# Optimization experiments

Measured on AMD Instinct MI355X. Metric: run time of the kernel, lower is better.

## Reference

```python
import jax, jax.numpy as jnp
import numpy as np

N_ENT = 50000
N_EDGE = 500000
H_DIM = 128
N_REL_TAB = 475  # 2*n_rel + 1


def setup_inputs() -> dict:
    key = jax.random.key(0)
    ks = jax.random.split(key, 8)
    scale = 1.0 / np.sqrt(H_DIM)
    return {
        "ent_emb": jax.random.normal(ks[0], (N_ENT, H_DIM), jnp.float32) * scale,
        "rel_emb": jax.random.normal(ks[1], (N_REL_TAB, H_DIM), jnp.float32) * scale,
        "w_edge": jax.random.normal(ks[2], (H_DIM, H_DIM), jnp.float32) * scale,
        "w_node": jax.random.normal(ks[3], (H_DIM, H_DIM), jnp.float32) * scale,
        "w_comp": jax.random.normal(ks[4], (H_DIM, H_DIM), jnp.float32) * scale,
        "src": jax.random.randint(ks[5], (N_EDGE,), 0, N_ENT, jnp.int32),
        "dst": jax.random.randint(ks[6], (N_EDGE,), 0, N_ENT, jnp.int32),
        "rel_id": jax.random.randint(ks[7], (N_EDGE,), 0, N_REL_TAB - 1, jnp.int32),
    }


def _edge_softmax(logits, dst, n_nodes):
    # dgl.ops.edge_softmax: softmax over incoming edges of each destination node
    m = jax.ops.segment_max(logits, dst, num_segments=n_nodes)  # (N,)
    ex = jnp.exp(logits - m[dst])                               # (E,)
    s = jax.ops.segment_sum(ex, dst, num_segments=n_nodes)     # (N,)
    return ex / s[dst]


def _attn_aggregate(msg, key_emb_dst, dst, n_nodes, w):
    # norm = e_dot_v, edge_softmax, weighted scatter-sum, GEMM, Tanh
    logits = jnp.sum(msg * key_emb_dst, axis=-1)                # (E,)
    a = _edge_softmax(logits, dst, n_nodes)                     # (E,)
    neigh = jax.ops.segment_sum(msg * a[:, None], dst, num_segments=n_nodes)  # (N,H)
    return jnp.tanh(neigh @ w)


def reference(ent_emb, rel_emb, w_edge, w_node, w_comp, src, dst, rel_id):
    n = ent_emb.shape[0]
    v = ent_emb[dst]            # (E,H) destination node emb (shared key for all layers)
    u = ent_emb[src]            # (E,H)
    r = rel_emb[rel_id]         # (E,H)

    # EdgeLayer: message = rel emb
    edge_out = _attn_aggregate(r, v, dst, n, w_edge)
    # NodeLayer: message = src node emb (u_dot_v logits, u_mul_e aggregation)
    node_out = _attn_aggregate(u, v, dst, n, w_node)
    # CompLayer (comp_op='add'): message = u + rel emb
    comp_out = _attn_aggregate(u + r, v, dst, n, w_comp)

    return ent_emb + edge_out + node_out + comp_out
```

## Files before the change

### kernel.cpp

```cpp
#include <hip/hip_runtime.h>
#include <math.h>

#define N_ENT   50000
#define N_EDGE  500000
#define HD      128

typedef unsigned int u32;
typedef __attribute__((ext_vector_type(8))) short short8;
typedef __attribute__((ext_vector_type(4))) float f32x4;
typedef __attribute__((ext_vector_type(4))) u32 u32x4;

__device__ __forceinline__ u32 bf16_1(float f) {
  u32 u = __float_as_uint(f);
  return (u + 0x7fffu + ((u >> 16) & 1u)) >> 16;
}
__device__ __forceinline__ u32 bf16_pack(float lo, float hi) {
  return bf16_1(lo) | (bf16_1(hi) << 16);
}
__device__ __forceinline__ float fast_tanh(float x) {
  float e = __expf(2.f * x);
  return 1.f - 2.f * __builtin_amdgcn_rcpf(e + 1.f);
}

__global__ void k_degree(const int* __restrict__ dst, int* __restrict__ counts) {
  int e = blockIdx.x * 256 + threadIdx.x;
  if (e < N_EDGE) atomicAdd(&counts[dst[e]], 1);
}

__global__ void k_blocksum(const int* __restrict__ counts, int* __restrict__ bsum) {
  __shared__ int sh[256];
  int i = blockIdx.x * 256 + threadIdx.x;
  sh[threadIdx.x] = (i < N_ENT) ? counts[i] : 0;
  __syncthreads();
  for (int off = 128; off > 0; off >>= 1) {
    if (threadIdx.x < off) sh[threadIdx.x] += sh[threadIdx.x + off];
    __syncthreads();
  }
  if (threadIdx.x == 0) bsum[blockIdx.x] = sh[0];
}

__global__ void k_scan_top(int* __restrict__ bsum, int nb) {
  __shared__ int sh[256];
  int t = threadIdx.x;
  int v = (t < nb) ? bsum[t] : 0;
  sh[t] = v;
  __syncthreads();
  for (int off = 1; off < 256; off <<= 1) {
    int x = (t >= off) ? sh[t - off] : 0;
    __syncthreads();
    sh[t] += x;
    __syncthreads();
  }
  if (t < nb) bsum[t] = sh[t] - v;
}

__global__ void k_scan_final(const int* __restrict__ counts, const int* __restrict__ bsum,
                             int* __restrict__ row_ptr) {
  __shared__ int sh[256];
  int t = threadIdx.x;
  int i = blockIdx.x * 256 + t;
  int v = (i < N_ENT) ? counts[i] : 0;
  sh[t] = v;
  __syncthreads();
  for (int off = 1; off < 256; off <<= 1) {
    int x = (t >= off) ? sh[t - off] : 0;
    __syncthreads();
    sh[t] += x;
    __syncthreads();
  }
  if (i < N_ENT) row_ptr[i] = sh[t] - v + bsum[blockIdx.x];
  if (i == N_ENT - 1) row_ptr[N_ENT] = N_EDGE;
}

__global__ void k_scatter(const int* __restrict__ src, const int* __restrict__ dst,
                          const int* __restrict__ rel, const int* __restrict__ row_ptr,
                          int* __restrict__ cursor, int2* __restrict__ psr) {
  int e = blockIdx.x * 256 + threadIdx.x;
  if (e >= N_EDGE) return;
  int d = dst[e];
  int pos = row_ptr[d] + atomicAdd(&cursor[d], 1);
  psr[pos] = make_int2(src[e], rel[e]);
}

__global__ __launch_bounds__(256) void k_aggregate(
    const float* __restrict__ ent, const float* __restrict__ rel,
    const int* __restrict__ row_ptr, const int2* __restrict__ psr,
    u32* __restrict__ neighb) {
  int lane = threadIdx.x & 63;
  int node = blockIdx.x * 4 + (threadIdx.x >> 6);
  int grp = lane >> 4, gl = lane & 15;

  const float* vp = ent + (size_t)node * HD + gl * 8;
  float4 va = *(const float4*)vp, vb = *(const float4*)(vp + 4);
  float vv[8] = {va.x, va.y, va.z, va.w, vb.x, vb.y, vb.z, vb.w};

  float S0 = 0.f, S1 = 0.f, S2 = 0.f;
  float a0[8], a1[8], a2[8];
#pragma unroll
  for (int j = 0; j < 8; ++j) a0[j] = a1[j] = a2[j] = 0.f;

  int e0 = row_ptr[node], e1 = row_ptr[node + 1];
  if (e0 < e1) {
    int elast = e1 - 1;
    int ep = e0 + grp;
    int ec = (ep < e1) ? ep : elast;
    int2 sr = psr[ec];
    const float* up = ent + (size_t)sr.x * HD + gl * 8;
    const float* rp = rel + (size_t)sr.y * HD + gl * 8;
    float4 uA = *(const float4*)up, uB = *(const float4*)(up + 4);
    float4 rA = *(const float4*)rp, rB = *(const float4*)(rp + 4);

    for (int eb = e0; eb < e1; eb += 4) {
      float cu[8] = {uA.x, uA.y, uA.z, uA.w, uB.x, uB.y, uB.z, uB.w};
      float cr[8] = {rA.x, rA.y, rA.z, rA.w, rB.x, rB.y, rB.z, rB.w};
      bool valid = (eb + grp < e1);

      if (eb + 4 < e1) {
        int en = eb + 4 + grp;
        int ecn = (en < e1) ? en : elast;
        int2 srn = psr[ecn];
        const float* upn = ent + (size_t)srn.x * HD + gl * 8;
        const float* rpn = rel + (size_t)srn.y * HD + gl * 8;
        uA = *(const float4*)upn; uB = *(const float4*)(upn + 4);
        rA = *(const float4*)rpn; rB = *(const float4*)(rpn + 4);
      }

      float pu = 0.f, pq = 0.f;
#pragma unroll
      for (int j = 0; j < 8; ++j) {
        pu = fmaf(cu[j], vv[j], pu);
        pq = fmaf(cr[j], vv[j], pq);
      }
#pragma unroll
      for (int off = 1; off < 16; off <<= 1) {
        pu += __shfl_xor(pu, off, 64);
        pq += __shfl_xor(pq, off, 64);
      }
      float e_u = valid ? __expf(pu) : 0.f;
      float e_r = valid ? __expf(pq) : 0.f;
      float e_c = e_u * e_r;
      S0 += e_r; S1 += e_u; S2 += e_c;
#pragma unroll
      for (int j = 0; j < 8; ++j) {
        a0[j] = fmaf(e_r, cr[j], a0[j]);
        a1[j] = fmaf(e_u, cu[j], a1[j]);
        a2[j] = fmaf(e_c, cu[j] + cr[j], a2[j]);
      }
    }
  }

  S0 += __shfl_xor(S0, 16, 64); S0 += __shfl_xor(S0, 32, 64);
  S1 += __shfl_xor(S1, 16, 64); S1 += __shfl_xor(S1, 32, 64);
  S2 += __shfl_xor(S2, 16, 64); S2 += __shfl_xor(S2, 32, 64);
  float w0 = (S0 > 0.f) ? __builtin_amdgcn_rcpf(S0) : 0.f;
  float w1 = (S1 > 0.f) ? __builtin_amdgcn_rcpf(S1) : 0.f;
  float w2 = (S2 > 0.f) ? __builtin_amdgcn_rcpf(S2) : 0.f;
#pragma unroll
  for (int j = 0; j < 8; ++j) {
    a0[j] += __shfl_xor(a0[j], 16, 64); a0[j] += __shfl_xor(a0[j], 32, 64);
    a1[j] += __shfl_xor(a1[j], 16, 64); a1[j] += __shfl_xor(a1[j], 32, 64);
    a2[j] += __shfl_xor(a2[j], 16, 64); a2[j] += __shfl_xor(a2[j], 32, 64);
  }

  int base = node * 64 + gl * 4;
  if (grp == 0) {
    u32x4 o = {bf16_pack(a0[0] * w0, a0[1] * w0), bf16_pack(a0[2] * w0, a0[3] * w0),
               bf16_pack(a0[4] * w0, a0[5] * w0), bf16_pack(a0[6] * w0, a0[7] * w0)};
    *(u32x4*)(neighb + base) = o;
  } else if (grp == 1) {
    u32x4 o = {bf16_pack(a1[0] * w1, a1[1] * w1), bf16_pack(a1[2] * w1, a1[3] * w1),
               bf16_pack(a1[4] * w1, a1[5] * w1), bf16_pack(a1[6] * w1, a1[7] * w1)};
    *(u32x4*)(neighb + N_ENT * 64 + base) = o;
  } else if (grp == 2) {
    u32x4 o = {bf16_pack(a2[0] * w2, a2[1] * w2), bf16_pack(a2[2] * w2, a2[3] * w2),
               bf16_pack(a2[4] * w2, a2[5] * w2), bf16_pack(a2[6] * w2, a2[7] * w2)};
    *(u32x4*)(neighb + 2 * N_ENT * 64 + base) = o;
  }
}

__global__ void k_pack(const float* __restrict__ we, const float* __restrict__ wn,
                       const float* __restrict__ wc, u32* __restrict__ wpack) {
  int idx = blockIdx.x * 256 + threadIdx.x;
  if (idx >= 3 * 8 * 4 * 64) return;
  int lane = idx & 63, ks = (idx >> 6) & 3, ct = (idx >> 8) & 7, l = idx >> 11;
  const float* W = (l == 0) ? we : (l == 1) ? wn : wc;
  int c = ct * 16 + (lane & 15);
  int kb = ks * 32 + (lane >> 4) * 8;
  u32x4 o;
#pragma unroll
  for (int jp = 0; jp < 4; ++jp) {
    int k0 = kb + 2 * jp;
    o[jp] = bf16_pack(W[k0 * HD + c], W[(k0 + 1) * HD + c]);
  }
  *(u32x4*)(wpack + idx * 4) = o;
}

__global__ __launch_bounds__(256) void k_out(
    const float* __restrict__ ent, const u32* __restrict__ neighb,
    const u32* __restrict__ wpack, float* __restrict__ out) {
  int lane = threadIdx.x & 63, wv = threadIdx.x >> 6;
  int n0 = blockIdx.x * 64 + wv * 16;

  int arow = n0 + (lane & 15);
  int arow_c = (arow < N_ENT) ? arow : 0;
  int ko2 = (lane >> 4) * 4;

  f32x4 res[8];
#pragma unroll
  for (int t = 0; t < 8; ++t) res[t] = (f32x4){0.f, 0.f, 0.f, 0.f};

#pragma unroll
  for (int l = 0; l < 3; ++l) {
    const u32* nb = neighb + (size_t)l * N_ENT * 64;
    short8 a[4];
#pragma unroll
    for (int ks = 0; ks < 4; ++ks)
      a[ks] = *(const short8*)(nb + (size_t)arow_c * 64 + ks * 16 + ko2);
    const u32* wp = wpack + l * 8192;
#pragma unroll
    for (int ct = 0; ct < 8; ++ct) {
      f32x4 acc = (f32x4){0.f, 0.f, 0.f, 0.f};
#pragma unroll
      for (int ks = 0; ks < 4; ++ks) {
        short8 b = *(const short8*)(wp + ((ct * 4 + ks) * 64 + lane) * 4);
        acc = __builtin_amdgcn_mfma_f32_16x16x32_bf16(a[ks], b, acc, 0, 0, 0);
      }
#pragma unroll
      for (int r = 0; r < 4; ++r) res[ct][r] += fast_tanh(acc[r]);
    }
  }
  int rbase = n0 + (lane >> 4) * 4;
  int cbase = lane & 15;
#pragma unroll
  for (int ct = 0; ct < 8; ++ct) {
    int col = ct * 16 + cbase;
#pragma unroll
    for (int r = 0; r < 4; ++r) {
      int row = rbase + r;
      if (row < N_ENT)
        out[(size_t)row * HD + col] = ent[(size_t)row * HD + col] + res[ct][r];
    }
  }
}

extern "C" void kernel_launch(void* const* d_in, const int* in_sizes, int n_in,
                              void* d_out, int out_size, void* d_ws, size_t ws_size,
                              hipStream_t stream) {
  const float* ent = (const float*)d_in[0];
  const float* rel = (const float*)d_in[1];
  const float* w_e = (const float*)d_in[2];
  const float* w_n = (const float*)d_in[3];
  const float* w_c = (const float*)d_in[4];
  const int* src = (const int*)d_in[5];
  const int* dst = (const int*)d_in[6];
  const int* relid = (const int*)d_in[7];
  float* out = (float*)d_out;

  char* ws = (char*)d_ws;
  size_t off = 0;
  auto alloc = [&](size_t bytes) {
    void* p = ws + off;
    off = (off + bytes + 255) & ~(size_t)255;
    return p;
  };
  int* counts = (int*)alloc((size_t)N_ENT * 4);
  int* cursor = (int*)alloc((size_t)N_ENT * 4);
  int* row_ptr = (int*)alloc((size_t)(N_ENT + 1) * 4);
  int* bsum = (int*)alloc(256 * 4);
  int2* psr = (int2*)alloc((size_t)N_EDGE * 8);
  u32* neighb = (u32*)alloc(3ull * N_ENT * 64 * 4);
  u32* wpack = (u32*)alloc((size_t)3 * 8 * 4 * 64 * 4 * 4);
  (void)ws_size; (void)in_sizes; (void)n_in; (void)out_size;

  hipMemsetAsync(counts, 0, (size_t)((char*)row_ptr - (char*)counts), stream);

  int nb = (N_ENT + 255) / 256;
  k_degree<<<(N_EDGE + 255) / 256, 256, 0, stream>>>(dst, counts);
  k_blocksum<<<nb, 256, 0, stream>>>(counts, bsum);
  k_scan_top<<<1, 256, 0, stream>>>(bsum, nb);
  k_scan_final<<<nb, 256, 0, stream>>>(counts, bsum, row_ptr);
  k_scatter<<<(N_EDGE + 255) / 256, 256, 0, stream>>>(src, dst, relid, row_ptr, cursor,
                                                      psr);
  k_pack<<<24, 256, 0, stream>>>(w_e, w_n, w_c, wpack);
  k_aggregate<<<N_ENT / 4, 256, 0, stream>>>(ent, rel, row_ptr, psr, neighb);
  k_out<<<(N_ENT + 63) / 64, 256, 0, stream>>>(ent, neighb, wpack, out);
}
```

Before: 249.9 us.

## Gather bf16 copies of embeddings with packed edge indices and deeper prefetch

Adds a conversion kernel that writes bf16 copies of the entity and relation embeddings, merged with the weight packing kernel. The aggregation kernel now gathers 16-byte bf16 rows instead of 32-byte fp32 rows, which halves the bytes moved on the random-access edge gather. The per-edge (src, rel) pair is packed into one 32-bit word, and the loop is double-buffered two edge groups ahead. The trade-off is an extra pass over the entity table, plus bf16 rounding of the messages and logits before exp, which may cost accuracy.

```diff
diff --git a/kernel.cpp b/kernel.cpp
--- a/kernel.cpp
+++ b/kernel.cpp
@@ -2,6 +2,7 @@
 #include <math.h>
 
 #define N_ENT   50000
+#define N_REL   475
 #define N_EDGE  500000
 #define HD      128
 
@@ -17,6 +18,8 @@
 __device__ __forceinline__ u32 bf16_pack(float lo, float hi) {
   return bf16_1(lo) | (bf16_1(hi) << 16);
 }
+__device__ __forceinline__ float bf_lo(u32 w) { return __uint_as_float(w << 16); }
+__device__ __forceinline__ float bf_hi(u32 w) { return __uint_as_float(w & 0xffff0000u); }
 __device__ __forceinline__ float fast_tanh(float x) {
   float e = __expf(2.f * x);
   return 1.f - 2.f * __builtin_amdgcn_rcpf(e + 1.f);
@@ -74,18 +77,56 @@
 
 __global__ void k_scatter(const int* __restrict__ src, const int* __restrict__ dst,
                           const int* __restrict__ rel, const int* __restrict__ row_ptr,
-                          int* __restrict__ cursor, int2* __restrict__ psr) {
+                          int* __restrict__ cursor, u32* __restrict__ psru) {
   int e = blockIdx.x * 256 + threadIdx.x;
   if (e >= N_EDGE) return;
   int d = dst[e];
   int pos = row_ptr[d] + atomicAdd(&cursor[d], 1);
-  psr[pos] = make_int2(src[e], rel[e]);
+  psru[pos] = (u32)src[e] | ((u32)rel[e] << 16);
+}
+
+__global__ void k_cvt_pack(const float* __restrict__ ent, const float* __restrict__ rel,
+                           const float* __restrict__ we, const float* __restrict__ wn,
+                           const float* __restrict__ wc, u32* __restrict__ ent16,
+                           u32* __restrict__ rel16, u32* __restrict__ wpack) {
+  const int CVT = (N_ENT + N_REL) * 16;
+  int t = blockIdx.x * 256 + threadIdx.x;
+  if (t < CVT) {
+    int row = t >> 4, seg = t & 15;
+    const float* s;
+    u32* d;
+    if (row < N_ENT) {
+      s = ent + (size_t)row * HD + seg * 8;
+      d = ent16 + (size_t)row * 64 + seg * 4;
+    } else {
+      int rr = row - N_ENT;
+      s = rel + (size_t)rr * HD + seg * 8;
+      d = rel16 + (size_t)rr * 64 + seg * 4;
+    }
+    float4 A = *(const float4*)s, B = *(const float4*)(s + 4);
+    u32x4 o = {bf16_pack(A.x, A.y), bf16_pack(A.z, A.w),
+               bf16_pack(B.x, B.y), bf16_pack(B.z, B.w)};
+    *(u32x4*)d = o;
+  } else if (t < CVT + 3 * 8 * 4 * 64) {
+    int idx = t - CVT;
+    int lane = idx & 63, ks = (idx >> 6) & 3, ct = (idx >> 8) & 7, l = idx >> 11;
+    const float* W = (l == 0) ? we : (l == 1) ? wn : wc;
+    int c = ct * 16 + (lane & 15);
+    int kb = ks * 32 + (lane >> 4) * 8;
+    u32x4 o;
+#pragma unroll
+    for (int jp = 0; jp < 4; ++jp) {
+      int k0 = kb + 2 * jp;
+      o[jp] = bf16_pack(W[k0 * HD + c], W[(k0 + 1) * HD + c]);
+    }
+    *(u32x4*)(wpack + idx * 4) = o;
+  }
 }
 
 __global__ __launch_bounds__(256) void k_aggregate(
-    const float* __restrict__ ent, const float* __restrict__ rel,
-    const int* __restrict__ row_ptr, const int2* __restrict__ psr,
-    u32* __restrict__ neighb) {
+    const float* __restrict__ ent, const u32* __restrict__ ent16,
+    const u32* __restrict__ rel16, const int* __restrict__ row_ptr,
+    const u32* __restrict__ psru, u32* __restrict__ neighb) {
   int lane = threadIdx.x & 63;
   int node = blockIdx.x * 4 + (threadIdx.x >> 6);
   int grp = lane >> 4, gl = lane & 15;
@@ -102,29 +143,21 @@
   int e0 = row_ptr[node], e1 = row_ptr[node + 1];
   if (e0 < e1) {
     int elast = e1 - 1;
-    int ep = e0 + grp;
-    int ec = (ep < e1) ? ep : elast;
-    int2 sr = psr[ec];
-    const float* up = ent + (size_t)sr.x * HD + gl * 8;
-    const float* rp = rel + (size_t)sr.y * HD + gl * 8;
-    float4 uA = *(const float4*)up, uB = *(const float4*)(up + 4);
-    float4 rA = *(const float4*)rp, rB = *(const float4*)(rp + 4);
-
-    for (int eb = e0; eb < e1; eb += 4) {
-      float cu[8] = {uA.x, uA.y, uA.z, uA.w, uB.x, uB.y, uB.z, uB.w};
-      float cr[8] = {rA.x, rA.y, rA.z, rA.w, rB.x, rB.y, rB.z, rB.w};
+    auto fetch = [&](int eb, u32x4& U, u32x4& R) {
+      int e = eb + grp;
+      u32 p = psru[(e < e1) ? e : elast];
+      U = *(const u32x4*)(ent16 + (size_t)(p & 0xFFFFu) * 64 + gl * 4);
+      R = *(const u32x4*)(rel16 + (size_t)(p >> 16) * 64 + gl * 4);
+    };
+    auto process = [&](u32x4& U, u32x4& R, int eb) {
+      float cu[8], cr[8];
+#pragma unroll
+      for (int k = 0; k < 4; ++k) {
+        cu[2 * k] = bf_lo(U[k]); cu[2 * k + 1] = bf_hi(U[k]);
+        cr[2 * k] = bf_lo(R[k]); cr[2 * k + 1] = bf_hi(R[k]);
+      }
+      if (eb + 8 < e1) fetch(eb + 8, U, R);
       bool valid = (eb + grp < e1);
-
-      if (eb + 4 < e1) {
-        int en = eb + 4 + grp;
-        int ecn = (en < e1) ? en : elast;
-        int2 srn = psr[ecn];
-        const float* upn = ent + (size_t)srn.x * HD + gl * 8;
-        const float* rpn = rel + (size_t)srn.y * HD + gl * 8;
-        uA = *(const float4*)upn; uB = *(const float4*)(upn + 4);
-        rA = *(const float4*)rpn; rB = *(const float4*)(rpn + 4);
-      }
-
       float pu = 0.f, pq = 0.f;
 #pragma unroll
       for (int j = 0; j < 8; ++j) {
@@ -146,6 +179,13 @@
         a1[j] = fmaf(e_u, cu[j], a1[j]);
         a2[j] = fmaf(e_c, cu[j] + cr[j], a2[j]);
       }
+    };
+    u32x4 uA, rA, uB, rB;
+    fetch(e0, uA, rA);
+    if (e0 + 4 < e1) fetch(e0 + 4, uB, rB);
+    for (int eb = e0; eb < e1; eb += 8) {
+      process(uA, rA, eb);
+      if (eb + 4 < e1) process(uB, rB, eb + 4);
     }
   }
 
@@ -178,23 +218,6 @@
   }
 }
 
-__global__ void k_pack(const float* __restrict__ we, const float* __restrict__ wn,
-                       const float* __restrict__ wc, u32* __restrict__ wpack) {
-  int idx = blockIdx.x * 256 + threadIdx.x;
-  if (idx >= 3 * 8 * 4 * 64) return;
-  int lane = idx & 63, ks = (idx >> 6) & 3, ct = (idx >> 8) & 7, l = idx >> 11;
-  const float* W = (l == 0) ? we : (l == 1) ? wn : wc;
-  int c = ct * 16 + (lane & 15);
-  int kb = ks * 32 + (lane >> 4) * 8;
-  u32x4 o;
-#pragma unroll
-  for (int jp = 0; jp < 4; ++jp) {
-    int k0 = kb + 2 * jp;
-    o[jp] = bf16_pack(W[k0 * HD + c], W[(k0 + 1) * HD + c]);
-  }
-  *(u32x4*)(wpack + idx * 4) = o;
-}
-
 __global__ __launch_bounds__(256) void k_out(
     const float* __restrict__ ent, const u32* __restrict__ neighb,
     const u32* __restrict__ wpack, float* __restrict__ out) {
@@ -267,7 +290,9 @@
   int* cursor = (int*)alloc((size_t)N_ENT * 4);
   int* row_ptr = (int*)alloc((size_t)(N_ENT + 1) * 4);
   int* bsum = (int*)alloc(256 * 4);
-  int2* psr = (int2*)alloc((size_t)N_EDGE * 8);
+  u32* psru = (u32*)alloc((size_t)N_EDGE * 4);
+  u32* ent16 = (u32*)alloc((size_t)N_ENT * 64 * 4);
+  u32* rel16 = (u32*)alloc((size_t)N_REL * 64 * 4);
   u32* neighb = (u32*)alloc(3ull * N_ENT * 64 * 4);
   u32* wpack = (u32*)alloc((size_t)3 * 8 * 4 * 64 * 4 * 4);
   (void)ws_size; (void)in_sizes; (void)n_in; (void)out_size;
@@ -280,8 +305,10 @@
   k_scan_top<<<1, 256, 0, stream>>>(bsum, nb);
   k_scan_final<<<nb, 256, 0, stream>>>(counts, bsum, row_ptr);
   k_scatter<<<(N_EDGE + 255) / 256, 256, 0, stream>>>(src, dst, relid, row_ptr, cursor,
-                                                      psr);
-  k_pack<<<24, 256, 0, stream>>>(w_e, w_n, w_c, wpack);
-  k_aggregate<<<N_ENT / 4, 256, 0, stream>>>(ent, rel, row_ptr, psr, neighb);
+                                                      psru);
+  const int CVTN = (N_ENT + N_REL) * 16 + 3 * 8 * 4 * 64;
+  k_cvt_pack<<<(CVTN + 255) / 256, 256, 0, stream>>>(ent, rel, w_e, w_n, w_c, ent16,
+                                                     rel16, wpack);
+  k_aggregate<<<N_ENT / 4, 256, 0, stream>>>(ent, ent16, rel16, row_ptr, psru, neighb);
   k_out<<<(N_ENT + 63) / 64, 256, 0, stream>>>(ent, neighb, wpack, out);
 }
```

Result: no change. 245.2 us (-1.9%).
